# Performance work log

Hardware: AMD Instinct MI355X
Metric: run time of the kernel (lower is better)

The kernel has to match this reference:

```python
import jax, jax.numpy as jnp
import numpy as np

N_NODES = 100000   # graph size N
DIM     = 128      # embedding dim d
M_SEL   = 4096     # selected nodes per forward
N_POS   = 32       # positives per node (padded/fixed sample of pos_neigh)
N_NEG   = 256      # negatives per node (fixed sample of neg_samples)


def setup_inputs() -> dict:
    key = jax.random.key(0)
    ks = jax.random.split(key, 8)
    return {
        "P": jax.random.normal(ks[0], (N_NODES, DIM), dtype=jnp.float32),
        "W_d": jax.random.normal(ks[1], (DIM,), dtype=jnp.float32),
        "deg_vec": jax.random.uniform(ks[2], (N_NODES,), dtype=jnp.float32) * 64.0,
        "nodes": jax.random.randint(ks[3], (M_SEL,), 0, N_NODES),
        "pos_idx": jax.random.randint(ks[4], (M_SEL, N_POS), 0, N_NODES),
        "neg_idx": jax.random.randint(ks[5], (M_SEL, N_NEG), 0, N_NODES),
        "deg_pos_idx": jax.random.randint(ks[6], (M_SEL, N_POS), 0, N_NODES),
        "deg_neg_idx": jax.random.randint(ks[7], (M_SEL, N_NEG), 0, N_NODES),
    }


def my_sigmoid(x):
    # Sigmoid_alt: sign-carrying sigmoid in (-1, 1) (parity used in the repo's plots)
    return 2.0 * jax.nn.sigmoid(x) - 1.0


def _contrast(Z, nodes, pos_idx, neg_idx):
    # softmax_formula vectorized over the selected-node batch:
    #   loss_i = -( mean_p hamming(Z_i, Z_p) - log sum_n exp(hamming(Z_i, Z_n)) )
    Zi = Z[nodes]                                            # [M, d]
    h_pos = jnp.abs(Zi[:, None, :] - Z[pos_idx]).sum(-1)    # [M, P]
    h_neg = jnp.abs(Zi[:, None, :] - Z[neg_idx]).sum(-1)    # [M, K]
    log_sum_neg = jax.scipy.special.logsumexp(h_neg, axis=1)  # stable log(sum(exp(.)))
    per_node = log_sum_neg - h_pos.mean(axis=1)
    return per_node.sum()


def reference(P, W_d, deg_vec, nodes, pos_idx, neg_idx, deg_pos_idx, deg_neg_idx):
    Z = my_sigmoid(P)                                        # [N, d]
    # degree_loss: MSE(Z @ W_d, deg_vec)
    L_deg = jnp.mean((Z @ W_d - deg_vec) ** 2)
    # contrast_adj_n_degDist: adjacency and degree-distribution contrastive totals
    L_adj = _contrast(Z, nodes, pos_idx, neg_idx)
    L_deg_dist = _contrast(Z, nodes, deg_pos_idx, deg_neg_idx)
    return (L_adj, L_deg_dist, L_deg)
```

## Files before the change

### kernel.cpp

```cpp
#include <hip/hip_runtime.h>
#include <math.h>

#define N_NODES_C 100000
#define DIM_C     128
#define M_SEL_C   4096
#define N_POS_C   32
#define N_NEG_C   256
#define QSCALE    (2.0f / 255.0f)

__device__ __forceinline__ float wsum64(float v) {
#pragma unroll
    for (int o = 32; o; o >>= 1) v += __shfl_xor(v, o, 64);
    return v;
}
__device__ __forceinline__ float wmax64(float v) {
#pragma unroll
    for (int o = 32; o; o >>= 1) v = fmaxf(v, __shfl_xor(v, o, 64));
    return v;
}
__device__ __forceinline__ float hsum32(float v) {
#pragma unroll
    for (int o = 1; o < 32; o <<= 1) v += __shfl_xor(v, o, 64);
    return v;
}
__device__ __forceinline__ int gsum8(int v) {
#pragma unroll
    for (int o = 1; o < 8; o <<= 1) v += __shfl_xor(v, o, 64);
    return v;
}

__device__ __forceinline__ unsigned sad8(unsigned a, unsigned b, unsigned acc) {
    unsigned d;
    asm volatile("v_sad_u8 %0, %1, %2, %3" : "=v"(d) : "v"(a), "v"(b), "v"(acc));
    return d;
}

__global__ void k_zero(float* out, int n) {
    int i = blockIdx.x * blockDim.x + threadIdx.x;
    if (i < n) out[i] = 0.0f;
}

__global__ __launch_bounds__(256) void k_z_deg(
    const float* __restrict__ P, const float* __restrict__ Wd,
    const float* __restrict__ deg, unsigned* __restrict__ Q,
    float* __restrict__ out)
{
    const int lane = threadIdx.x & 63;
    const int sl   = lane & 31;
    const int hi   = lane >> 5;
    const int wv   = threadIdx.x >> 6;
    const int gw   = blockIdx.x * 4 + wv;
    const int nw   = gridDim.x * 4;
    const float4 w = *(const float4*)(Wd + 4 * sl);
    float acc = 0.0f;
    for (int pr = gw; pr < N_NODES_C / 2; pr += nw) {
        const int row = 2 * pr + hi;
        float4 p = *(const float4*)(P + (size_t)row * DIM_C + 4 * sl);
        float r0 = __fdividef(255.0f, 1.0f + __expf(-p.x));
        float r1 = __fdividef(255.0f, 1.0f + __expf(-p.y));
        float r2 = __fdividef(255.0f, 1.0f + __expf(-p.z));
        float r3 = __fdividef(255.0f, 1.0f + __expf(-p.w));
        unsigned q = __float2uint_rn(r0) | (__float2uint_rn(r1) << 8) |
                     (__float2uint_rn(r2) << 16) | (__float2uint_rn(r3) << 24);
        Q[(size_t)row * (DIM_C / 4) + sl] = q;
        float z0 = fmaf(r0, QSCALE, -1.0f), z1 = fmaf(r1, QSCALE, -1.0f);
        float z2 = fmaf(r2, QSCALE, -1.0f), z3 = fmaf(r3, QSCALE, -1.0f);
        float d4 = fmaf(z0, w.x, fmaf(z1, w.y, fmaf(z2, w.z, z3 * w.w)));
        d4 = hsum32(d4);
        if (sl == 0) { float d = d4 - deg[row]; acc = fmaf(d, d, acc); }
    }
    __shared__ float part[4];
    float a = wsum64(acc);
    if (lane == 0) part[wv] = a;
    __syncthreads();
    if (threadIdx.x == 0)
        atomicAdd(out + 2, (part[0] + part[1] + part[2] + part[3]) * (1.0f / N_NODES_C));
}

__global__ __launch_bounds__(256) void k_contrast(
    const unsigned* __restrict__ Q,
    const int* __restrict__ nodes,
    const int* __restrict__ pos_a, const int* __restrict__ neg_a,
    const int* __restrict__ pos_b, const int* __restrict__ neg_b,
    float* __restrict__ out)
{
    const int bid = blockIdx.x;
    const int m   = bid & (M_SEL_C - 1);
    const int sel = bid >> 12;
    const int* __restrict__ pos_idx = sel ? pos_b : pos_a;
    const int* __restrict__ neg_idx = sel ? neg_b : neg_a;

    const int tid  = threadIdx.x;
    const int lane = tid & 63;
    const int wv   = tid >> 6;
    const int g    = lane >> 3;
    const int l8   = lane & 7;

    __shared__ int  sNeg[N_NEG_C];
    __shared__ int  sPos[N_POS_C];
    __shared__ int  hneg[N_NEG_C];
    __shared__ int  pp[4];
    __shared__ float rmax[4];
    __shared__ float rsum[4];

    sNeg[tid] = neg_idx[m * N_NEG_C + tid];
    if (tid < N_POS_C) sPos[tid] = pos_idx[m * N_POS_C + tid];
    const int node = nodes[m];
    uint4 c = *(const uint4*)(Q + (size_t)node * (DIM_C / 4) + l8 * 4);
    __syncthreads();

    {
        int j = wv * 8 + g;
        int n = sPos[j];
        uint4 b = *(const uint4*)(Q + (size_t)n * (DIM_C / 4) + l8 * 4);
        int s = (int)sad8(c.w, b.w, sad8(c.z, b.z, sad8(c.y, b.y, sad8(c.x, b.x, 0u))));
#pragma unroll
        for (int o = 1; o < 64; o <<= 1) s += __shfl_xor(s, o, 64);
        if (lane == 0) pp[wv] = s;
    }

#pragma unroll 4
    for (int t = 0; t < 8; ++t) {
        int j = (t * 4 + wv) * 8 + g;
        int n = sNeg[j];
        uint4 b = *(const uint4*)(Q + (size_t)n * (DIM_C / 4) + l8 * 4);
        int s = (int)sad8(c.w, b.w, sad8(c.z, b.z, sad8(c.y, b.y, sad8(c.x, b.x, 0u))));
        s = gsum8(s);
        if (l8 == 0) hneg[j] = s;
    }
    __syncthreads();

    float v  = (float)hneg[tid] * QSCALE;
    float mx = wmax64(v);
    if (lane == 0) rmax[wv] = mx;
    __syncthreads();
    float gmax = fmaxf(fmaxf(rmax[0], rmax[1]), fmaxf(rmax[2], rmax[3]));
    float s = wsum64(__expf(v - gmax));
    if (lane == 0) rsum[wv] = s;
    __syncthreads();

    if (tid == 0) {
        float tot = rsum[0] + rsum[1] + rsum[2] + rsum[3];
        float lse = gmax + __logf(tot);
        float pm  = (float)(pp[0] + pp[1] + pp[2] + pp[3]) * QSCALE * (1.0f / N_POS_C);
        atomicAdd(out + sel, lse - pm);
    }
}

extern "C" void kernel_launch(void* const* d_in, const int* in_sizes, int n_in,
                              void* d_out, int out_size, void* d_ws, size_t ws_size,
                              hipStream_t stream) {
    const float* P    = (const float*)d_in[0];
    const float* Wd   = (const float*)d_in[1];
    const float* deg  = (const float*)d_in[2];
    const int* nodes  = (const int*)d_in[3];
    const int* pos_i  = (const int*)d_in[4];
    const int* neg_i  = (const int*)d_in[5];
    const int* dpos_i = (const int*)d_in[6];
    const int* dneg_i = (const int*)d_in[7];
    float* out  = (float*)d_out;
    unsigned* Q = (unsigned*)d_ws;

    k_zero<<<1, 256, 0, stream>>>(out, out_size);
    k_z_deg<<<1024, 256, 0, stream>>>(P, Wd, deg, Q, out);
    k_contrast<<<2 * M_SEL_C, 256, 0, stream>>>(
        Q, nodes, pos_i, neg_i, dpos_i, dneg_i, out);
}
```

Baseline: 234.4 us.

## Assign one wavefront per selected node with online logsumexp and batched gathers

The contrast kernel now processes one (node, set) pair per wavefront instead of per 256-thread block. Each wave keeps a running max/sum for the logsumexp in registers and merges across lane groups with shuffles. This removes the shared-memory histogram and the block barriers, and issues 8 gathers at a time to increase memory-level parallelism. The z/degree kernel grid is also doubled. The cost is more register pressure and extra exp calls in the online softmax.

Result: slower. 242.0 us (+3.2%).

```diff
diff --git a/kernel.cpp b/kernel.cpp
--- a/kernel.cpp
+++ b/kernel.cpp
@@ -11,11 +11,6 @@
 __device__ __forceinline__ float wsum64(float v) {
 #pragma unroll
     for (int o = 32; o; o >>= 1) v += __shfl_xor(v, o, 64);
-    return v;
-}
-__device__ __forceinline__ float wmax64(float v) {
-#pragma unroll
-    for (int o = 32; o; o >>= 1) v = fmaxf(v, __shfl_xor(v, o, 64));
     return v;
 }
 __device__ __forceinline__ float hsum32(float v) {
@@ -33,6 +28,9 @@
     unsigned d;
     asm volatile("v_sad_u8 %0, %1, %2, %3" : "=v"(d) : "v"(a), "v"(b), "v"(acc));
     return d;
+}
+__device__ __forceinline__ int sad16B(uint4 a, uint4 b) {
+    return (int)sad8(a.w, b.w, sad8(a.z, b.z, sad8(a.y, b.y, sad8(a.x, b.x, 0u))));
 }
 
 __global__ void k_zero(float* out, int n) {
@@ -77,72 +75,79 @@
         atomicAdd(out + 2, (part[0] + part[1] + part[2] + part[3]) * (1.0f / N_NODES_C));
 }
 
-__global__ __launch_bounds__(256) void k_contrast(
+__global__ __launch_bounds__(256, 6) void k_contrast(
     const unsigned* __restrict__ Q,
     const int* __restrict__ nodes,
     const int* __restrict__ pos_a, const int* __restrict__ neg_a,
     const int* __restrict__ pos_b, const int* __restrict__ neg_b,
     float* __restrict__ out)
 {
-    const int bid = blockIdx.x;
-    const int m   = bid & (M_SEL_C - 1);
-    const int sel = bid >> 12;
+    const int tid  = threadIdx.x;
+    const int wv   = tid >> 6;
+    const int lane = tid & 63;
+    const int l8   = lane & 7;
+    const int g    = lane >> 3;
+
+    const int id   = blockIdx.x * 4 + wv;
+    const int sel  = id >> 12;
+    const int m    = id & (M_SEL_C - 1);
     const int* __restrict__ pos_idx = sel ? pos_b : pos_a;
     const int* __restrict__ neg_idx = sel ? neg_b : neg_a;
 
-    const int tid  = threadIdx.x;
-    const int lane = tid & 63;
-    const int wv   = tid >> 6;
-    const int g    = lane >> 3;
-    const int l8   = lane & 7;
+    __shared__ int sNeg[4][N_NEG_C];
+    __shared__ int sPos[4][N_POS_C];
 
-    __shared__ int  sNeg[N_NEG_C];
-    __shared__ int  sPos[N_POS_C];
-    __shared__ int  hneg[N_NEG_C];
-    __shared__ int  pp[4];
-    __shared__ float rmax[4];
-    __shared__ float rsum[4];
-
-    sNeg[tid] = neg_idx[m * N_NEG_C + tid];
-    if (tid < N_POS_C) sPos[tid] = pos_idx[m * N_POS_C + tid];
+    ((int4*)sNeg[wv])[lane] = ((const int4*)(neg_idx + m * N_NEG_C))[lane];
+    if (lane < N_POS_C / 4)
+        ((int4*)sPos[wv])[lane] = ((const int4*)(pos_idx + m * N_POS_C))[lane];
     const int node = nodes[m];
-    uint4 c = *(const uint4*)(Q + (size_t)node * (DIM_C / 4) + l8 * 4);
+    const uint4* __restrict__ Q4 = (const uint4*)Q;
+    uint4 c = Q4[((unsigned)node << 3) + l8];
     __syncthreads();
 
+    float ps = 0.0f;
     {
-        int j = wv * 8 + g;
-        int n = sPos[j];
-        uint4 b = *(const uint4*)(Q + (size_t)n * (DIM_C / 4) + l8 * 4);
-        int s = (int)sad8(c.w, b.w, sad8(c.z, b.z, sad8(c.y, b.y, sad8(c.x, b.x, 0u))));
+        int pn[4];
 #pragma unroll
-        for (int o = 1; o < 64; o <<= 1) s += __shfl_xor(s, o, 64);
-        if (lane == 0) pp[wv] = s;
+        for (int t = 0; t < 4; ++t) pn[t] = sPos[wv][t * 8 + g];
+        uint4 pb[4];
+#pragma unroll
+        for (int t = 0; t < 4; ++t) pb[t] = Q4[((unsigned)pn[t] << 3) + l8];
+#pragma unroll
+        for (int t = 0; t < 4; ++t) ps += (float)gsum8(sad16B(c, pb[t]));
     }
 
-#pragma unroll 4
-    for (int t = 0; t < 8; ++t) {
-        int j = (t * 4 + wv) * 8 + g;
-        int n = sNeg[j];
-        uint4 b = *(const uint4*)(Q + (size_t)n * (DIM_C / 4) + l8 * 4);
-        int s = (int)sad8(c.w, b.w, sad8(c.z, b.z, sad8(c.y, b.y, sad8(c.x, b.x, 0u))));
-        s = gsum8(s);
-        if (l8 == 0) hneg[j] = s;
+    float mx = -1e30f, sm = 0.0f;
+#pragma unroll 1
+    for (int tt = 0; tt < 32; tt += 8) {
+        int nn[8];
+#pragma unroll
+        for (int u = 0; u < 8; ++u) nn[u] = sNeg[wv][(tt + u) * 8 + g];
+        uint4 nb[8];
+#pragma unroll
+        for (int u = 0; u < 8; ++u) nb[u] = Q4[((unsigned)nn[u] << 3) + l8];
+#pragma unroll
+        for (int u = 0; u < 8; ++u) {
+            float v = (float)gsum8(sad16B(c, nb[u])) * QSCALE;
+            float nm = fmaxf(mx, v);
+            sm = fmaf(sm, __expf(mx - nm), __expf(v - nm));
+            mx = nm;
+        }
     }
-    __syncthreads();
 
-    float v  = (float)hneg[tid] * QSCALE;
-    float mx = wmax64(v);
-    if (lane == 0) rmax[wv] = mx;
-    __syncthreads();
-    float gmax = fmaxf(fmaxf(rmax[0], rmax[1]), fmaxf(rmax[2], rmax[3]));
-    float s = wsum64(__expf(v - gmax));
-    if (lane == 0) rsum[wv] = s;
-    __syncthreads();
+#pragma unroll
+    for (int o = 8; o < 64; o <<= 1) {
+        float om = __shfl_xor(mx, o, 64);
+        float os = __shfl_xor(sm, o, 64);
+        float nm = fmaxf(mx, om);
+        sm = fmaf(sm, __expf(mx - nm), os * __expf(om - nm));
+        mx = nm;
+        ps += __shfl_xor(ps, o, 64);
+    }
 
-    if (tid == 0) {
-        float tot = rsum[0] + rsum[1] + rsum[2] + rsum[3];
-        float lse = gmax + __logf(tot);
-        float pm  = (float)(pp[0] + pp[1] + pp[2] + pp[3]) * QSCALE * (1.0f / N_POS_C);
+    if (lane == 0) {
+        float lse = mx + __logf(sm);
+        float pm  = ps * QSCALE * (1.0f / N_POS_C);
         atomicAdd(out + sel, lse - pm);
     }
 }
@@ -162,7 +167,7 @@
     unsigned* Q = (unsigned*)d_ws;
 
     k_zero<<<1, 256, 0, stream>>>(out, out_size);
-    k_z_deg<<<1024, 256, 0, stream>>>(P, Wd, deg, Q, out);
-    k_contrast<<<2 * M_SEL_C, 256, 0, stream>>>(
+    k_z_deg<<<2048, 256, 0, stream>>>(P, Wd, deg, Q, out);
+    k_contrast<<<2048, 256, 0, stream>>>(
         Q, nodes, pos_i, neg_i, dpos_i, dneg_i, out);
 }
```
